# Optimization experiments

Hardware: AMD Instinct MI355X
Metric: run time of the kernel (lower is better)

The kernel has to match this reference:

```python
import jax, jax.numpy as jnp
import numpy as np
from jax import lax


def _conv(x, w, pad):
    # NCHW / OIHW conv, stride 1
    return lax.conv_general_dilated(
        x, w, window_strides=(1, 1), padding=((pad, pad), (pad, pad)),
        dimension_numbers=("NCHW", "OIHW", "NCHW"))


def setup_inputs() -> dict:
    key = jax.random.key(0)
    k1, k2, k3, k4 = jax.random.split(key, 4)
    B, C, H, W = 16, 64, 128, 128
    OUT = 64
    x = jax.random.normal(k1, (B, C, H, W), jnp.float32)
    w_off = jax.random.normal(k2, (2 * C, C, 3, 3), jnp.float32) * 0.01  # offset conv, init std 0.01
    w_conv = jax.random.normal(k3, (OUT, C, 3, 3), jnp.float32) * 0.05
    b_conv = jax.random.normal(k4, (OUT,), jnp.float32) * 0.01
    return {"x": x, "w_off": w_off, "w_conv": w_conv, "b_conv": b_conv}


def _deform(x, w_off):
    B, C, H, W = x.shape
    off = _conv(x, w_off, 1)                      # (B, 2C, H, W)
    # Faithful to torch .view(-1, H, W, 2): raw row-major memory reinterpretation
    off = off.reshape(B * C, H * W, 2)            # (BC, HW, 2) -> (row_off, col_off)
    gr, gc = jnp.meshgrid(jnp.arange(H), jnp.arange(W), indexing="ij")
    grid = jnp.stack([gr.reshape(-1), gc.reshape(-1)], -1).astype(x.dtype)  # (HW, 2)
    coords = off + grid                           # (BC, HW, 2)
    rows = jnp.clip(coords[..., 0], 0, H - 1)
    cols = jnp.clip(coords[..., 1], 0, W - 1)
    r0 = jnp.floor(rows); r1 = jnp.ceil(rows)
    c0 = jnp.floor(cols); c1 = jnp.ceil(cols)
    xf = x.reshape(B * C, H * W)

    def gather(r, c):
        idx = lax.stop_gradient((r * W + c).astype(jnp.int32))
        return jnp.take_along_axis(xf, idx, axis=1)

    v_lt = gather(r0, c0)   # (floor row, floor col)
    v_rb = gather(r1, c1)   # (ceil row,  ceil col)
    v_lb = gather(r0, c1)   # (floor row, ceil col)
    v_rt = gather(r1, c0)   # (ceil row,  floor col)
    fr = rows - r0
    fc = cols - c0
    vals_t = fr * (v_rt - v_lt) + v_lt
    vals_b = fr * (v_rb - v_lb) + v_lb
    mapped = fc * (vals_b - vals_t) + vals_t      # (BC, HW)
    return mapped.reshape(B, C, H, W)


def reference(x, w_off, w_conv, b_conv):
    xd = _deform(x, w_off)
    return _conv(xd, w_conv, 1) + b_conv[None, :, None, None]
```

## Files before the change

### kernel.cpp

```cpp
#include <hip/hip_runtime.h>

typedef _Float16 f16;
typedef _Float16 half8 __attribute__((ext_vector_type(8)));
typedef _Float16 f16x2 __attribute__((ext_vector_type(2)));
typedef float f32x4 __attribute__((ext_vector_type(4)));
typedef int i32x4 __attribute__((ext_vector_type(4)));
typedef unsigned short ushort_t;


__global__ __launch_bounds__(256) void transpose_pack_k(
    const float* __restrict__ x, f16* __restrict__ xT,
    const float* __restrict__ w_off, const float* __restrict__ w_conv,
    f16* __restrict__ W1p, f16* __restrict__ W2p)
{
    __shared__ float lds[64 * 132];
    const int tid = threadIdx.x;
    if (blockIdx.x >= 2048) {
        for (int t = (blockIdx.x - 2048) * 256 + tid; t < 110592; t += 16384) {
            if (t < 73728) {
                int tap = t >> 13, oc = (t >> 6) & 127, ic = t & 63;
                W1p[t] = (f16)w_off[(oc * 64 + ic) * 9 + tap];
            } else {
                int t2 = t - 73728;
                int tap = t2 >> 12, oc = (t2 >> 6) & 63, ic = t2 & 63;
                W2p[t2] = (f16)w_conv[(oc * 64 + ic) * 9 + tap];
            }
        }
        return;
    }
    const int b = blockIdx.x >> 7, h = blockIdx.x & 127;
    const float4* x4 = (const float4*)x;
    for (int i = tid; i < 2048; i += 256) {
        int ic = i >> 5, wq = i & 31;
        float4 v = x4[(b * 64 + ic) * 4096 + h * 32 + wq];
        *(float4*)&lds[ic * 132 + wq * 4] = v;
    }
    __syncthreads();
    for (int i = tid; i < 1024; i += 256) {
        int w = i & 127, kg = i >> 7;
        half8 hv;
        #pragma unroll
        for (int j = 0; j < 8; ++j) hv[j] = (f16)lds[(kg * 8 + j) * 132 + w];
        *(half8*)&xT[(((size_t)(b * 128 + h) * 128 + w) << 6) + kg * 8] = hv;
    }
}

__device__ __forceinline__ float bilin(const float* __restrict__ xp, float rr, float cc) {
    rr = fminf(fmaxf(rr, 0.f), 127.f);
    cc = fminf(fmaxf(cc, 0.f), 127.f);
    const float r0f = floorf(rr), c0f = floorf(cc);
    const float r1f = ceilf(rr),  c1f = ceilf(cc);
    const int r0 = (int)r0f, r1 = (int)r1f, c0 = (int)c0f, c1 = (int)c1f;
    const float v_lt = xp[(r0 << 7) + c0];
    const float v_rt = xp[(r1 << 7) + c0];
    const float v_lb = xp[(r0 << 7) + c1];
    const float v_rb = xp[(r1 << 7) + c1];
    const float fr = rr - r0f, fc = cc - c0f;
    const float vt = fr * (v_rt - v_lt) + v_lt;
    const float vb = fr * (v_rb - v_lb) + v_lb;
    return fc * (vb - vt) + vt;
}

__global__ __launch_bounds__(256, 4) void conv1_deform_k(
    const f16* __restrict__ xT, const float* __restrict__ x,
    const f16* __restrict__ Wp, f16* __restrict__ mapped)
{
    __shared__ char lds[25344];
    ushort_t* cres = (ushort_t*)lds;

    const int tid = threadIdx.x;
    const int sr = blockIdx.x >> 1, ph = blockIdx.x & 1;
    const int b = blockIdx.y;
    const int t = sr >> 1, u = sr & 1;
    const int col0 = ph * 64;

    {
        const i32x4* s4 = (const i32x4*)xT;
        for (int s = tid; s < 1584; s += 256) {
            int kg = s & 7, q = s >> 3;
            int c = q % 66, r = q / 66;
            int rowg = sr + r - 1, wg = col0 + c - 1;
            i32x4 v = {0, 0, 0, 0};
            if ((unsigned)rowg < 128u && (unsigned)wg < 128u)
                v = s4[((b * 128 + rowg) * 128 + wg) * 8 + kg];
            int off = (q << 7) + (kg << 4);
            off ^= (c & 7) << 4;
            *(i32x4*)(lds + off) = v;
        }
    }
    __syncthreads();

    const int lane = tid & 63, wv = tid >> 6;
    const int l15 = lane & 15, l4 = lane >> 4;
    const int ocb = wv * 32 + l15;

    f32x4 acc[2][4];
    #pragma unroll
    for (int m = 0; m < 2; ++m)
        #pragma unroll
        for (int n = 0; n < 4; ++n) acc[m][n] = {0.f, 0.f, 0.f, 0.f};

    half8 a_cur[2], a_nxt[2];
    #pragma unroll
    for (int m = 0; m < 2; ++m)
        a_cur[m] = *(const half8*)&Wp[(0 * 128 + ocb + m * 16) * 64 + l4 * 8];

    #pragma unroll
    for (int step = 0; step < 18; ++step) {
        const int tap = step >> 1, ks = step & 1;
        const int ky = tap / 3, kx = tap % 3;
        if (step < 17) {
            const int tap1 = (step + 1) >> 1, ks1 = (step + 1) & 1;
            #pragma unroll
            for (int m = 0; m < 2; ++m)
                a_nxt[m] = *(const half8*)&Wp[(tap1 * 128 + ocb + m * 16) * 64 + ks1 * 32 + l4 * 8];
        }
        #pragma unroll
        for (int n = 0; n < 4; ++n) {
            const int c = n * 16 + l15 + kx;
            int off = ((ky * 66 + c) << 7) + (ks << 6) + (l4 << 4);
            off ^= (c & 7) << 4;
            const half8 bf = *(const half8*)(lds + off);
            acc[0][n] = __builtin_amdgcn_mfma_f32_16x16x32_f16(a_cur[0], bf, acc[0][n], 0, 0, 0);
            acc[1][n] = __builtin_amdgcn_mfma_f32_16x16x32_f16(a_cur[1], bf, acc[1][n], 0, 0, 0);
        }
        #pragma unroll
        for (int m = 0; m < 2; ++m) a_cur[m] = a_nxt[m];
    }

    __syncthreads();

    #pragma unroll
    for (int m = 0; m < 2; ++m) {
        const int oc0 = wv * 32 + m * 16 + l4 * 4;
        #pragma unroll
        for (int n = 0; n < 4; ++n) {
            const int pix = n * 16 + l15;
            const int base = pix * 130 + oc0;
            f16x2 p0; p0[0] = (f16)acc[m][n][0]; p0[1] = (f16)acc[m][n][1];
            f16x2 p1; p1[0] = (f16)acc[m][n][2]; p1[1] = (f16)acc[m][n][3];
            *(f16x2*)&cres[base]     = p0;
            *(f16x2*)&cres[base + 2] = p1;
        }
    }
    __syncthreads();

    {
        const int w_rel = tid & 31;
        const int hsel = (tid >> 5) & 1;
        const int cg = tid >> 6;
        const int w_out = u * 64 + 32 * ph + w_rel;
        const int h_out = t + hsel * 64;
        const int q = 2 * w_rel;
        const float hb = (float)h_out, wb = (float)w_out;
        f16* mp = mapped + ((((size_t)b << 14) + h_out * 128 + w_out) << 6) + cg * 16;

        #pragma unroll
        for (int j = 0; j < 2; ++j) {
            half8 ov;
            #pragma unroll
            for (int e = 0; e < 8; ++e) {
                const int c = cg * 16 + j * 8 + e;
                const float R  = (float)*(const f16*)&cres[q * 130 + 2 * c + hsel];
                const float Cf = (float)*(const f16*)&cres[(q + 1) * 130 + 2 * c + hsel];
                const float* xp = x + (((size_t)b * 64 + c) << 14);
                ov[e] = (f16)bilin(xp, R + hb, Cf + wb);
            }
            *(half8*)&mp[j * 8] = ov;
        }
    }
}

__global__ __launch_bounds__(256, 6) void conv2_k(
    const f16* __restrict__ src, const f16* __restrict__ Wp,
    const float* __restrict__ bias, float* __restrict__ out)
{
    __shared__ char lds[25344];
    const int tid = threadIdx.x;
    const int h = blockIdx.x >> 1, ph = blockIdx.x & 1;
    const int b = blockIdx.y;
    const int col0 = ph * 64;

    {
        const i32x4* s4 = (const i32x4*)src;
        for (int s = tid; s < 1584; s += 256) {
            int kg = s & 7, q = s >> 3;
            int c = q % 66, r = q / 66;
            int rowg = h + r - 1, wg = col0 + c - 1;
            i32x4 v = {0, 0, 0, 0};
            if ((unsigned)rowg < 128u && (unsigned)wg < 128u)
                v = s4[((b * 128 + rowg) * 128 + wg) * 8 + kg];
            int off = (q << 7) + (kg << 4);
            off ^= (c & 7) << 4;
            *(i32x4*)(lds + off) = v;
        }
    }
    __syncthreads();

    const int lane = tid & 63, wv = tid >> 6;
    const int l15 = lane & 15, l4 = lane >> 4;
    const int wm = wv >> 1, wn = wv & 1;
    const int ocb = wm * 32 + l15;
    const int pixb = wn * 32;

    f32x4 acc[2][2];
    #pragma unroll
    for (int m = 0; m < 2; ++m)
        #pragma unroll
        for (int n = 0; n < 2; ++n) acc[m][n] = {0.f, 0.f, 0.f, 0.f};

    half8 a_cur[2], a_nxt[2];
    #pragma unroll
    for (int m = 0; m < 2; ++m)
        a_cur[m] = *(const half8*)&Wp[(0 * 64 + ocb + m * 16) * 64 + l4 * 8];

    #pragma unroll
    for (int step = 0; step < 18; ++step) {
        const int tap = step >> 1, ks = step & 1;
        const int ky = tap / 3, kx = tap % 3;
        if (step < 17) {
            const int tap1 = (step + 1) >> 1, ks1 = (step + 1) & 1;
            #pragma unroll
            for (int m = 0; m < 2; ++m)
                a_nxt[m] = *(const half8*)&Wp[(tap1 * 64 + ocb + m * 16) * 64 + ks1 * 32 + l4 * 8];
        }
        #pragma unroll
        for (int n = 0; n < 2; ++n) {
            const int c = pixb + n * 16 + l15 + kx;
            int off = ((ky * 66 + c) << 7) + (ks << 6) + (l4 << 4);
            off ^= (c & 7) << 4;
            const half8 bf = *(const half8*)(lds + off);
            acc[0][n] = __builtin_amdgcn_mfma_f32_16x16x32_f16(a_cur[0], bf, acc[0][n], 0, 0, 0);
            acc[1][n] = __builtin_amdgcn_mfma_f32_16x16x32_f16(a_cur[1], bf, acc[1][n], 0, 0, 0);
        }
        #pragma unroll
        for (int m = 0; m < 2; ++m) a_cur[m] = a_nxt[m];
    }

    #pragma unroll
    for (int m = 0; m < 2; ++m) {
        #pragma unroll
        for (int i = 0; i < 4; ++i) {
            const int oc = wm * 32 + m * 16 + l4 * 4 + i;
            const float bb = bias[oc];
            #pragma unroll
            for (int n = 0; n < 2; ++n) {
                const int pix = col0 + pixb + n * 16 + l15;
                out[(((size_t)b * 64 + oc) << 14) + h * 128 + pix] = acc[m][n][i] + bb;
            }
        }
    }
}

extern "C" void kernel_launch(void* const* d_in, const int* in_sizes, int n_in,
                              void* d_out, int out_size, void* d_ws, size_t ws_size,
                              hipStream_t stream) {
    const float* x      = (const float*)d_in[0];
    const float* w_off  = (const float*)d_in[1];
    const float* w_conv = (const float*)d_in[2];
    const float* b_conv = (const float*)d_in[3];
    float* out = (float*)d_out;

    char* ws = (char*)d_ws;
    f16* xT     = (f16*)ws;
    f16* mapped = (f16*)(ws + 33554432);
    f16* W1p    = (f16*)(ws + 67108864);
    f16* W2p    = (f16*)(ws + 67108864 + 147456);

    transpose_pack_k<<<2112, 256, 0, stream>>>(x, xT, w_off, w_conv, W1p, W2p);
    conv1_deform_k<<<dim3(256, 16), 256, 0, stream>>>(xT, x, W1p, mapped);
    conv2_k<<<dim3(256, 16), 256, 0, stream>>>(mapped, W2p, b_conv, out);
}
```

Measured before the change: 315.5 us.

## Stream multiple rows per block with rolling LDS row buffer in both convs

Both conv kernels now process several consecutive output rows per block, holding a 4-slot ring of input rows in LDS so each input row is loaded once instead of three times. The next row is prefetched into registers during the MFMA loop, and weights use a 3-deep register pipeline. In conv1 the bilinear gather for the previous row is interleaved with the current row's compute. Grids shrink to 256 and 512 blocks with larger LDS footprints, which lowers occupancy and parallelism on a large GPU.

```diff
diff --git a/kernel.cpp b/kernel.cpp
--- a/kernel.cpp
+++ b/kernel.cpp
@@ -61,136 +61,55 @@
     return fc * (vb - vt) + vt;
 }
 
-__global__ __launch_bounds__(256, 4) void conv1_deform_k(
+__device__ __forceinline__ void do_gather(
+    const char* lds, const float* __restrict__ x, f16* __restrict__ mapped,
+    int b, int srp, int tid)
+{
+    const ushort_t* cres = (const ushort_t*)(lds + 66560);
+    const int t = srp >> 1, u = srp & 1;
+    const int w_rel = tid & 63;
+    const int hsel = (tid >> 6) & 1;
+    const int cg = tid >> 7;
+    const int w_out = u * 64 + w_rel;
+    const int h_out = t + hsel * 64;
+    const int q = 2 * w_rel;
+    const float hb = (float)h_out, wb = (float)w_out;
+    f16* mp = mapped + ((((size_t)b << 14) + h_out * 128 + w_out) << 6) + cg * 16;
+
+    #pragma unroll
+    for (int jj = 0; jj < 2; ++jj) {
+        half8 ov;
+        #pragma unroll
+        for (int e = 0; e < 8; ++e) {
+            const int c = cg * 16 + jj * 8 + e;
+            const float R  = (float)*(const f16*)&cres[q * 130 + 2 * c + hsel];
+            const float Cf = (float)*(const f16*)&cres[(q + 1) * 130 + 2 * c + hsel];
+            const float* xp = x + (((size_t)b * 64 + c) << 14);
+            ov[e] = (f16)bilin(xp, R + hb, Cf + wb);
+        }
+        *(half8*)&mp[jj * 8] = ov;
+    }
+}
+
+__global__ __launch_bounds__(512, 2) void conv1_deform_k(
     const f16* __restrict__ xT, const float* __restrict__ x,
     const f16* __restrict__ Wp, f16* __restrict__ mapped)
 {
-    __shared__ char lds[25344];
-    ushort_t* cres = (ushort_t*)lds;
-
+    __shared__ char lds[99840];
     const int tid = threadIdx.x;
-    const int sr = blockIdx.x >> 1, ph = blockIdx.x & 1;
+    const int sr0 = blockIdx.x * 8;
     const int b = blockIdx.y;
-    const int t = sr >> 1, u = sr & 1;
-    const int col0 = ph * 64;
-
-    {
-        const i32x4* s4 = (const i32x4*)xT;
-        for (int s = tid; s < 1584; s += 256) {
-            int kg = s & 7, q = s >> 3;
-            int c = q % 66, r = q / 66;
-            int rowg = sr + r - 1, wg = col0 + c - 1;
+    const i32x4* s4 = (const i32x4*)xT;
+
+    for (int r = 0; r < 3; ++r) {
+        const int g = sr0 - 1 + r;
+        const int slotb = ((g + 4) & 3) * 16640;
+        for (int s = tid; s < 1040; s += 512) {
+            const int kg = s & 7, c = s >> 3, wg = c - 1;
             i32x4 v = {0, 0, 0, 0};
-            if ((unsigned)rowg < 128u && (unsigned)wg < 128u)
-                v = s4[((b * 128 + rowg) * 128 + wg) * 8 + kg];
-            int off = (q << 7) + (kg << 4);
-            off ^= (c & 7) << 4;
-            *(i32x4*)(lds + off) = v;
-        }
-    }
-    __syncthreads();
-
-    const int lane = tid & 63, wv = tid >> 6;
-    const int l15 = lane & 15, l4 = lane >> 4;
-    const int ocb = wv * 32 + l15;
-
-    f32x4 acc[2][4];
-    #pragma unroll
-    for (int m = 0; m < 2; ++m)
-        #pragma unroll
-        for (int n = 0; n < 4; ++n) acc[m][n] = {0.f, 0.f, 0.f, 0.f};
-
-    half8 a_cur[2], a_nxt[2];
-    #pragma unroll
-    for (int m = 0; m < 2; ++m)
-        a_cur[m] = *(const half8*)&Wp[(0 * 128 + ocb + m * 16) * 64 + l4 * 8];
-
-    #pragma unroll
-    for (int step = 0; step < 18; ++step) {
-        const int tap = step >> 1, ks = step & 1;
-        const int ky = tap / 3, kx = tap % 3;
-        if (step < 17) {
-            const int tap1 = (step + 1) >> 1, ks1 = (step + 1) & 1;
-            #pragma unroll
-            for (int m = 0; m < 2; ++m)
-                a_nxt[m] = *(const half8*)&Wp[(tap1 * 128 + ocb + m * 16) * 64 + ks1 * 32 + l4 * 8];
-        }
-        #pragma unroll
-        for (int n = 0; n < 4; ++n) {
-            const int c = n * 16 + l15 + kx;
-            int off = ((ky * 66 + c) << 7) + (ks << 6) + (l4 << 4);
-            off ^= (c & 7) << 4;
-            const half8 bf = *(const half8*)(lds + off);
-            acc[0][n] = __builtin_amdgcn_mfma_f32_16x16x32_f16(a_cur[0], bf, acc[0][n], 0, 0, 0);
-            acc[1][n] = __builtin_amdgcn_mfma_f32_16x16x32_f16(a_cur[1], bf, acc[1][n], 0, 0, 0);
-        }
-        #pragma unroll
-        for (int m = 0; m < 2; ++m) a_cur[m] = a_nxt[m];
-    }
-
-    __syncthreads();
-
-    #pragma unroll
-    for (int m = 0; m < 2; ++m) {
-        const int oc0 = wv * 32 + m * 16 + l4 * 4;
-        #pragma unroll
-        for (int n = 0; n < 4; ++n) {
-            const int pix = n * 16 + l15;
-            const int base = pix * 130 + oc0;
-            f16x2 p0; p0[0] = (f16)acc[m][n][0]; p0[1] = (f16)acc[m][n][1];
-            f16x2 p1; p1[0] = (f16)acc[m][n][2]; p1[1] = (f16)acc[m][n][3];
-            *(f16x2*)&cres[base]     = p0;
-            *(f16x2*)&cres[base + 2] = p1;
-        }
-    }
-    __syncthreads();
-
-    {
-        const int w_rel = tid & 31;
-        const int hsel = (tid >> 5) & 1;
-        const int cg = tid >> 6;
-        const int w_out = u * 64 + 32 * ph + w_rel;
-        const int h_out = t + hsel * 64;
-        const int q = 2 * w_rel;
-        const float hb = (float)h_out, wb = (float)w_out;
-        f16* mp = mapped + ((((size_t)b << 14) + h_out * 128 + w_out) << 6) + cg * 16;
-
-        #pragma unroll
-        for (int j = 0; j < 2; ++j) {
-            half8 ov;
-            #pragma unroll
-            for (int e = 0; e < 8; ++e) {
-                const int c = cg * 16 + j * 8 + e;
-                const float R  = (float)*(const f16*)&cres[q * 130 + 2 * c + hsel];
-                const float Cf = (float)*(const f16*)&cres[(q + 1) * 130 + 2 * c + hsel];
-                const float* xp = x + (((size_t)b * 64 + c) << 14);
-                ov[e] = (f16)bilin(xp, R + hb, Cf + wb);
-            }
-            *(half8*)&mp[j * 8] = ov;
-        }
-    }
-}
-
-__global__ __launch_bounds__(256, 6) void conv2_k(
-    const f16* __restrict__ src, const f16* __restrict__ Wp,
-    const float* __restrict__ bias, float* __restrict__ out)
-{
-    __shared__ char lds[25344];
-    const int tid = threadIdx.x;
-    const int h = blockIdx.x >> 1, ph = blockIdx.x & 1;
-    const int b = blockIdx.y;
-    const int col0 = ph * 64;
-
-    {
-        const i32x4* s4 = (const i32x4*)src;
-        for (int s = tid; s < 1584; s += 256) {
-            int kg = s & 7, q = s >> 3;
-            int c = q % 66, r = q / 66;
-            int rowg = h + r - 1, wg = col0 + c - 1;
-            i32x4 v = {0, 0, 0, 0};
-            if ((unsigned)rowg < 128u && (unsigned)wg < 128u)
-                v = s4[((b * 128 + rowg) * 128 + wg) * 8 + kg];
-            int off = (q << 7) + (kg << 4);
+            if ((unsigned)g < 128u && (unsigned)wg < 128u)
+                v = s4[((b * 128 + g) * 128 + wg) * 8 + kg];
+            int off = slotb + (c << 7) + (kg << 4);
             off ^= (c & 7) << 4;
             *(i32x4*)(lds + off) = v;
         }
@@ -201,54 +120,243 @@
     const int l15 = lane & 15, l4 = lane >> 4;
     const int wm = wv >> 1, wn = wv & 1;
     const int ocb = wm * 32 + l15;
-    const int pixb = wn * 32;
-
-    f32x4 acc[2][2];
-    #pragma unroll
-    for (int m = 0; m < 2; ++m)
-        #pragma unroll
-        for (int n = 0; n < 2; ++n) acc[m][n] = {0.f, 0.f, 0.f, 0.f};
-
-    half8 a_cur[2], a_nxt[2];
-    #pragma unroll
-    for (int m = 0; m < 2; ++m)
-        a_cur[m] = *(const half8*)&Wp[(0 * 64 + ocb + m * 16) * 64 + l4 * 8];
-
-    #pragma unroll
-    for (int step = 0; step < 18; ++step) {
-        const int tap = step >> 1, ks = step & 1;
-        const int ky = tap / 3, kx = tap % 3;
-        if (step < 17) {
-            const int tap1 = (step + 1) >> 1, ks1 = (step + 1) & 1;
+    const int pixb = wn * 64;
+    ushort_t* cres = (ushort_t*)(lds + 66560);
+
+    for (int i = 0; i < 8; ++i) {
+        const int sr = sr0 + i;
+        const int g = sr + 2;
+
+        i32x4 st0 = {0,0,0,0}, st1 = {0,0,0,0}, st2 = {0,0,0,0};
+        if (i < 7 && (unsigned)g < 128u) {
+            {
+                const int s = tid, kg = s & 7, c = s >> 3, wg = c - 1;
+                if ((unsigned)wg < 128u) st0 = s4[((b * 128 + g) * 128 + wg) * 8 + kg];
+            }
+            {
+                const int s = tid + 512, kg = s & 7, c = s >> 3, wg = c - 1;
+                if ((unsigned)wg < 128u) st1 = s4[((b * 128 + g) * 128 + wg) * 8 + kg];
+            }
+            if (tid < 16) {
+                const int s = tid + 1024, kg = s & 7, c = s >> 3, wg = c - 1;
+                if ((unsigned)wg < 128u) st2 = s4[((b * 128 + g) * 128 + wg) * 8 + kg];
+            }
+        }
+
+        f32x4 acc[2][4];
+        #pragma unroll
+        for (int m = 0; m < 2; ++m)
+            #pragma unroll
+            for (int n = 0; n < 4; ++n) acc[m][n] = {0.f, 0.f, 0.f, 0.f};
+
+        half8 ab[3][2];
+        #pragma unroll
+        for (int p = 0; p < 2; ++p)
             #pragma unroll
             for (int m = 0; m < 2; ++m)
-                a_nxt[m] = *(const half8*)&Wp[(tap1 * 64 + ocb + m * 16) * 64 + ks1 * 32 + l4 * 8];
-        }
-        #pragma unroll
-        for (int n = 0; n < 2; ++n) {
-            const int c = pixb + n * 16 + l15 + kx;
-            int off = ((ky * 66 + c) << 7) + (ks << 6) + (l4 << 4);
+                ab[p][m] = *(const half8*)&Wp[(0 * 128 + ocb + m * 16) * 64 + p * 32 + l4 * 8];
+
+        #pragma unroll
+        for (int step = 0; step < 18; ++step) {
+            const int tap = step >> 1, ks = step & 1;
+            const int ky = tap / 3, kx = tap % 3;
+            if (step < 16) {
+                const int s2 = step + 2, tap2 = s2 >> 1, ks2 = s2 & 1;
+                #pragma unroll
+                for (int m = 0; m < 2; ++m)
+                    ab[s2 % 3][m] = *(const half8*)&Wp[(tap2 * 128 + ocb + m * 16) * 64 + ks2 * 32 + l4 * 8];
+            }
+            const int slotb = ((sr - 1 + ky + 4) & 3) * 16640;
+            #pragma unroll
+            for (int n = 0; n < 4; ++n) {
+                const int c = pixb + n * 16 + l15 + kx;
+                int off = slotb + (c << 7) + (ks << 6) + (l4 << 4);
+                off ^= (c & 7) << 4;
+                const half8 bf = *(const half8*)(lds + off);
+                acc[0][n] = __builtin_amdgcn_mfma_f32_16x16x32_f16(ab[step % 3][0], bf, acc[0][n], 0, 0, 0);
+                acc[1][n] = __builtin_amdgcn_mfma_f32_16x16x32_f16(ab[step % 3][1], bf, acc[1][n], 0, 0, 0);
+            }
+        }
+
+        if (i < 7) {
+            const int slotb = ((g + 4) & 3) * 16640;
+            {
+                const int s = tid, kg = s & 7, c = s >> 3;
+                int off = slotb + (c << 7) + (kg << 4); off ^= (c & 7) << 4;
+                *(i32x4*)(lds + off) = st0;
+            }
+            {
+                const int s = tid + 512, kg = s & 7, c = s >> 3;
+                int off = slotb + (c << 7) + (kg << 4); off ^= (c & 7) << 4;
+                *(i32x4*)(lds + off) = st1;
+            }
+            if (tid < 16) {
+                const int s = tid + 1024, kg = s & 7, c = s >> 3;
+                int off = slotb + (c << 7) + (kg << 4); off ^= (c & 7) << 4;
+                *(i32x4*)(lds + off) = st2;
+            }
+        }
+
+        __syncthreads();
+        if (i > 0) do_gather(lds, x, mapped, b, sr - 1, tid);
+        __syncthreads();
+
+        #pragma unroll
+        for (int m = 0; m < 2; ++m) {
+            const int oc0 = wm * 32 + m * 16 + l4 * 4;
+            #pragma unroll
+            for (int n = 0; n < 4; ++n) {
+                const int pix = pixb + n * 16 + l15;
+                const int base = pix * 130 + oc0;
+                f16x2 p0; p0[0] = (f16)acc[m][n][0]; p0[1] = (f16)acc[m][n][1];
+                f16x2 p1; p1[0] = (f16)acc[m][n][2]; p1[1] = (f16)acc[m][n][3];
+                *(f16x2*)&cres[base]     = p0;
+                *(f16x2*)&cres[base + 2] = p1;
+            }
+        }
+    }
+    __syncthreads();
+    do_gather(lds, x, mapped, b, sr0 + 7, tid);
+}
+
+__global__ __launch_bounds__(256, 2) void conv2_k(
+    const f16* __restrict__ src, const f16* __restrict__ Wp,
+    const float* __restrict__ bias, float* __restrict__ out)
+{
+    __shared__ char lds[66560];
+    const int tid = threadIdx.x;
+    const int h0 = blockIdx.x * 4;
+    const int b = blockIdx.y;
+    const i32x4* s4 = (const i32x4*)src;
+
+    for (int r = 0; r < 3; ++r) {
+        const int g = h0 - 1 + r;
+        const int slotb = ((g + 4) & 3) * 16640;
+        for (int s = tid; s < 1040; s += 256) {
+            const int kg = s & 7, c = s >> 3, wg = c - 1;
+            i32x4 v = {0, 0, 0, 0};
+            if ((unsigned)g < 128u && (unsigned)wg < 128u)
+                v = s4[((b * 128 + g) * 128 + wg) * 8 + kg];
+            int off = slotb + (c << 7) + (kg << 4);
             off ^= (c & 7) << 4;
-            const half8 bf = *(const half8*)(lds + off);
-            acc[0][n] = __builtin_amdgcn_mfma_f32_16x16x32_f16(a_cur[0], bf, acc[0][n], 0, 0, 0);
-            acc[1][n] = __builtin_amdgcn_mfma_f32_16x16x32_f16(a_cur[1], bf, acc[1][n], 0, 0, 0);
-        }
-        #pragma unroll
-        for (int m = 0; m < 2; ++m) a_cur[m] = a_nxt[m];
-    }
-
-    #pragma unroll
-    for (int m = 0; m < 2; ++m) {
-        #pragma unroll
-        for (int i = 0; i < 4; ++i) {
-            const int oc = wm * 32 + m * 16 + l4 * 4 + i;
-            const float bb = bias[oc];
-            #pragma unroll
-            for (int n = 0; n < 2; ++n) {
-                const int pix = col0 + pixb + n * 16 + l15;
-                out[(((size_t)b * 64 + oc) << 14) + h * 128 + pix] = acc[m][n][i] + bb;
-            }
-        }
+            *(i32x4*)(lds + off) = v;
+        }
+    }
+    __syncthreads();
+
+    const int lane = tid & 63, wv = tid >> 6;
+    const int l15 = lane & 15, l4 = lane >> 4;
+    const int wm = wv >> 1, wn = wv & 1;
+    const int ocb = wm * 32 + l15;
+    const int pixb = wn * 64;
+
+    for (int i = 0; i < 4; ++i) {
+        const int h = h0 + i;
+        const int g = h + 2;
+
+        i32x4 st0 = {0,0,0,0}, st1 = {0,0,0,0}, st2 = {0,0,0,0}, st3 = {0,0,0,0}, st4 = {0,0,0,0};
+        if (i < 3 && (unsigned)g < 128u) {
+            {
+                const int s = tid, kg = s & 7, c = s >> 3, wg = c - 1;
+                if ((unsigned)wg < 128u) st0 = s4[((b * 128 + g) * 128 + wg) * 8 + kg];
+            }
+            {
+                const int s = tid + 256, kg = s & 7, c = s >> 3, wg = c - 1;
+                if ((unsigned)wg < 128u) st1 = s4[((b * 128 + g) * 128 + wg) * 8 + kg];
+            }
+            {
+                const int s = tid + 512, kg = s & 7, c = s >> 3, wg = c - 1;
+                if ((unsigned)wg < 128u) st2 = s4[((b * 128 + g) * 128 + wg) * 8 + kg];
+            }
+            {
+                const int s = tid + 768, kg = s & 7, c = s >> 3, wg = c - 1;
+                if ((unsigned)wg < 128u) st3 = s4[((b * 128 + g) * 128 + wg) * 8 + kg];
+            }
+            if (tid < 16) {
+                const int s = tid + 1024, kg = s & 7, c = s >> 3, wg = c - 1;
+                if ((unsigned)wg < 128u) st4 = s4[((b * 128 + g) * 128 + wg) * 8 + kg];
+            }
+        }
+
+        f32x4 acc[2][4];
+        #pragma unroll
+        for (int m = 0; m < 2; ++m)
+            #pragma unroll
+            for (int n = 0; n < 4; ++n) acc[m][n] = {0.f, 0.f, 0.f, 0.f};
+
+        half8 ab[3][2];
+        #pragma unroll
+        for (int p = 0; p < 2; ++p)
+            #pragma unroll
+            for (int m = 0; m < 2; ++m)
+                ab[p][m] = *(const half8*)&Wp[(0 * 64 + ocb + m * 16) * 64 + p * 32 + l4 * 8];
+
+        #pragma unroll
+        for (int step = 0; step < 18; ++step) {
+            const int tap = step >> 1, ks = step & 1;
+            const int ky = tap / 3, kx = tap % 3;
+            if (step < 16) {
+                const int s2 = step + 2, tap2 = s2 >> 1, ks2 = s2 & 1;
+                #pragma unroll
+                for (int m = 0; m < 2; ++m)
+                    ab[s2 % 3][m] = *(const half8*)&Wp[(tap2 * 64 + ocb + m * 16) * 64 + ks2 * 32 + l4 * 8];
+            }
+            const int slotb = ((h - 1 + ky + 4) & 3) * 16640;
+            #pragma unroll
+            for (int n = 0; n < 4; ++n) {
+                const int c = pixb + n * 16 + l15 + kx;
+                int off = slotb + (c << 7) + (ks << 6) + (l4 << 4);
+                off ^= (c & 7) << 4;
+                const half8 bf = *(const half8*)(lds + off);
+                acc[0][n] = __builtin_amdgcn_mfma_f32_16x16x32_f16(ab[step % 3][0], bf, acc[0][n], 0, 0, 0);
+                acc[1][n] = __builtin_amdgcn_mfma_f32_16x16x32_f16(ab[step % 3][1], bf, acc[1][n], 0, 0, 0);
+            }
+        }
+
+        if (i < 3) {
+            const int slotb = ((g + 4) & 3) * 16640;
+            {
+                const int s = tid, kg = s & 7, c = s >> 3;
+                int off = slotb + (c << 7) + (kg << 4); off ^= (c & 7) << 4;
+                *(i32x4*)(lds + off) = st0;
+            }
+            {
+                const int s = tid + 256, kg = s & 7, c = s >> 3;
+                int off = slotb + (c << 7) + (kg << 4); off ^= (c & 7) << 4;
+                *(i32x4*)(lds + off) = st1;
+            }
+            {
+                const int s = tid + 512, kg = s & 7, c = s >> 3;
+                int off = slotb + (c << 7) + (kg << 4); off ^= (c & 7) << 4;
+                *(i32x4*)(lds + off) = st2;
+            }
+            {
+                const int s = tid + 768, kg = s & 7, c = s >> 3;
+                int off = slotb + (c << 7) + (kg << 4); off ^= (c & 7) << 4;
+                *(i32x4*)(lds + off) = st3;
+            }
+            if (tid < 16) {
+                const int s = tid + 1024, kg = s & 7, c = s >> 3;
+                int off = slotb + (c << 7) + (kg << 4); off ^= (c & 7) << 4;
+                *(i32x4*)(lds + off) = st4;
+            }
+        }
+
+        #pragma unroll
+        for (int m = 0; m < 2; ++m) {
+            #pragma unroll
+            for (int j = 0; j < 4; ++j) {
+                const int oc = wm * 32 + m * 16 + l4 * 4 + j;
+                const float bb = bias[oc];
+                #pragma unroll
+                for (int n = 0; n < 4; ++n) {
+                    const int pix = pixb + n * 16 + l15;
+                    out[(((size_t)b * 64 + oc) << 14) + h * 128 + pix] = acc[m][n][j] + bb;
+                }
+            }
+        }
+
+        __syncthreads();
     }
 }
 
@@ -268,6 +376,6 @@
     f16* W2p    = (f16*)(ws + 67108864 + 147456);
 
     transpose_pack_k<<<2112, 256, 0, stream>>>(x, xT, w_off, w_conv, W1p, W2p);
-    conv1_deform_k<<<dim3(256, 16), 256, 0, stream>>>(xT, x, W1p, mapped);
-    conv2_k<<<dim3(256, 16), 256, 0, stream>>>(mapped, W2p, b_conv, out);
-}
+    conv1_deform_k<<<dim3(16, 16), 512, 0, stream>>>(xT, x, W1p, mapped);
+    conv2_k<<<dim3(32, 16), 256, 0, stream>>>(mapped, W2p, b_conv, out);
+}
```

Measured after the change: 282.2 us. 10.6% less time.
